# Kernel optimization log

Measured on AMD Instinct MI355X. Metric: run time of the kernel, lower is better.

## Reference

```python
import jax, jax.numpy as jnp
import numpy as np

B = 65536
DIM = 256       # latent_dim
N_EMBED = 1024  # codebook size


def setup_inputs() -> dict:
    key = jax.random.key(0)
    kx, ke = jax.random.split(key)
    x = jax.random.normal(kx, (B, DIM), dtype=jnp.float32)
    # rosinality Quantize stores codebook as embed[dim, n_embed]
    embed = jax.random.normal(ke, (DIM, N_EMBED), dtype=jnp.float32)
    return {"x": x, "embed": embed}


def reference(x, embed):
    # dist[b, k] = ||x_b||^2 - 2 x_b . e_k + ||e_k||^2  (negated for argmax in
    # the original; equivalent to argmin of the distance)
    x_sq = jnp.sum(x * x, axis=1, keepdims=True)            # [B, 1]
    e_sq = jnp.sum(embed * embed, axis=0, keepdims=True)    # [1, K]
    dist = x_sq - 2.0 * (x @ embed) + e_sq                  # [B, K]
    embed_ind = jnp.argmin(dist, axis=1)                    # [B] int
    # codebook lookup: embed.T is [K, dim]
    quantize = jnp.take(embed.T, embed_ind, axis=0)         # [B, dim]
    # commitment loss term
    diff = jnp.mean(jnp.square(jax.lax.stop_gradient(quantize) - x))
    # straight-through estimator
    quantize_st = x + jax.lax.stop_gradient(quantize - x)
    return quantize_st, diff, embed_ind
```

## Files before the change

kernel.cpp:

```cpp
#include <hip/hip_runtime.h>

#define NROWSQ   65536
#define NDIM     256
#define NCB      1024
#define DIFF_OFF 16777216
#define IDX_OFF  16777217

#define MARGIN_A 0.35f
#define MARGIN_A3 (MARGIN_A + 0.075f)
#define MARGIN_B 1.5e-3f
#define SCORE_SHIFT 384.0f

typedef __attribute__((ext_vector_type(8))) short s16x8;
typedef __attribute__((ext_vector_type(4))) float f32x4;

__device__ __forceinline__ unsigned short f2bf(float f) {
  union { float f; unsigned u; } v; v.f = f;
  return (unsigned short)((v.u + 0x7FFFu + ((v.u >> 16) & 1u)) >> 16);
}

__device__ __forceinline__ void gll16(const void* g, void* l) {
  __builtin_amdgcn_global_load_lds(
      (const __attribute__((address_space(1))) unsigned int*)g,
      (__attribute__((address_space(3))) unsigned int*)l, 16, 0, 0);
}

__device__ __forceinline__ void top2_merge(float& v1, int& i1, float& v2, int& i2,
                                           float ov1, int oi1, float ov2, int oi2) {
  if (ov1 > v1 || (ov1 == v1 && oi1 < i1)) {
    float nv2 = v1; int ni2 = i1;
    if (ov2 > nv2 || (ov2 == nv2 && oi2 < ni2)) { nv2 = ov2; ni2 = oi2; }
    v1 = ov1; i1 = oi1; v2 = nv2; i2 = ni2;
  } else if (ov1 > v2 || (ov1 == v2 && oi1 < i2)) {
    v2 = ov1; i2 = oi1;
  }
}

__device__ __forceinline__ float np_pairwise128(const float* p) {
  float r0 = p[0], r1 = p[1], r2 = p[2], r3 = p[3];
  float r4 = p[4], r5 = p[5], r6 = p[6], r7 = p[7];
  for (int i = 8; i < 128; i += 8) {
    r0 += p[i];     r1 += p[i + 1]; r2 += p[i + 2]; r3 += p[i + 3];
    r4 += p[i + 4]; r5 += p[i + 5]; r6 += p[i + 6]; r7 += p[i + 7];
  }
  return ((r0 + r1) + (r2 + r3)) + ((r4 + r5) + (r6 + r7));
}

__global__ void k0a_transpose(const float* __restrict__ E, float* __restrict__ embT,
                              unsigned short* __restrict__ cbT,
                              int* __restrict__ cnts, float* __restrict__ outDiff) {
  __shared__ float T[64][65];
  const int t = threadIdx.x;
  const int kbase = (blockIdx.x & 15) * 64;
  const int dbase = (blockIdx.x >> 4) * 64;
  if (blockIdx.x == 0) {
    if (t < 3) cnts[t] = 0;
    if (t == 3) *outDiff = 0.f;
  }
  #pragma unroll
  for (int i = 0; i < 4; ++i) {
    const int cid = i * 256 + t;
    const int dl = cid >> 4, kc = cid & 15;
    const float4 v = *(const float4*)(E + (size_t)(dbase + dl) * NCB + kbase + kc * 4);
    T[dl][kc * 4 + 0] = v.x; T[dl][kc * 4 + 1] = v.y;
    T[dl][kc * 4 + 2] = v.z; T[dl][kc * 4 + 3] = v.w;
  }
  __syncthreads();
  #pragma unroll
  for (int i = 0; i < 4; ++i) {
    const int cid = i * 256 + t;
    const int kl = cid >> 4, dc = cid & 15;
    float4 v;
    v.x = T[dc * 4 + 0][kl]; v.y = T[dc * 4 + 1][kl];
    v.z = T[dc * 4 + 2][kl]; v.w = T[dc * 4 + 3][kl];
    *(float4*)(embT + (size_t)(kbase + kl) * NDIM + dbase + dc * 4) = v;
    ushort4 b;
    b.x = f2bf(v.x); b.y = f2bf(v.y); b.z = f2bf(v.z); b.w = f2bf(v.w);
    const int dcol = dbase + dc * 4;
    const int sp = dcol ^ ((kl & 7) << 3);
    *(ushort4*)(cbT + (size_t)(kbase + kl) * NDIM + sp) = b;
  }
}

__global__ void k0b_esq(const float* __restrict__ embT, float* __restrict__ esq32,
                        float* __restrict__ esqs, float* __restrict__ esqr) {
  const int b = blockIdx.x, t = threadIdx.x;
  if (b < 128) {
    const int col = b * 8 + (t >> 5);
    const int l = t & 31;
    double s = 0.0;
    #pragma unroll
    for (int i = 0; i < 8; ++i) {
      const double v = (double)embT[(size_t)col * NDIM + l + i * 32];
      s += v * v;
    }
    #pragma unroll
    for (int m = 16; m >= 1; m >>= 1) s += __shfl_xor(s, m);
    if (l == 0) {
      esq32[col] = (float)(0.5 * s);
      esqs[col] = (float)(0.5 * s) - SCORE_SHIFT;
    }
  } else {
    __shared__ float Ls[16][260];
    const int col0 = (b - 128) * 16;
    #pragma unroll
    for (int i = 0; i < 4; ++i) {
      const int flat = i * 256 + t;
      const int row = flat >> 6, f4 = flat & 63;
      *(float4*)&Ls[row][f4 * 4] =
          *(const float4*)(embT + (size_t)(col0 + row) * NDIM + f4 * 4);
    }
    __syncthreads();
    if (t < 16) {
      float sr = 0.f;
      for (int d = 0; d < NDIM; ++d) {
        const float v = Ls[t][d];
        sr = sr + v * v;
      }
      esqr[col0 + t] = sr;
    }
  }
}

__global__ __launch_bounds__(256, 2) void k1_scores(
    const float* __restrict__ X, const unsigned short* __restrict__ cbT,
    const float* __restrict__ esqs, float* __restrict__ outIdx,
    int* __restrict__ cnts, int2* __restrict__ listP, int* __restrict__ listF) {
  __shared__ __align__(16) unsigned short Bs[2][64 * 256];
  __shared__ float esq_l[1024];
  const int t = threadIdx.x;
  const int lane = t & 63, w = t >> 6;
  const int l15 = lane & 15, quad = lane >> 4;
  const int rowbase = blockIdx.x * 128;
  const int swz = (l15 & 7) << 3;

  #pragma unroll
  for (int i = 0; i < 8; ++i)
    gll16(cbT + (size_t)(i * 256 + t) * 8, &Bs[0][(i * 256 + w * 64) * 8]);

  s16x8 afrag[2][8];
  #pragma unroll
  for (int m = 0; m < 2; ++m) {
    const float* xr = X + (size_t)(rowbase + w * 32 + m * 16 + l15) * NDIM;
    #pragma unroll
    for (int ks = 0; ks < 8; ++ks) {
      const float4 xa = *(const float4*)(xr + ks * 32 + quad * 8);
      const float4 xb = *(const float4*)(xr + ks * 32 + quad * 8 + 4);
      s16x8 a;
      a[0] = (short)f2bf(xa.x); a[1] = (short)f2bf(xa.y);
      a[2] = (short)f2bf(xa.z); a[3] = (short)f2bf(xa.w);
      a[4] = (short)f2bf(xb.x); a[5] = (short)f2bf(xb.y);
      a[6] = (short)f2bf(xb.z); a[7] = (short)f2bf(xb.w);
      afrag[m][ks] = a;
    }
  }

  {
    const float4 e4 = *(const float4*)(esqs + t * 4);
    *(float4*)(esq_l + t * 4) = e4;
  }

  int key1[2][4], key2[2][4], key3[2][4];
  #pragma unroll
  for (int m = 0; m < 2; ++m)
    #pragma unroll
    for (int r = 0; r < 4; ++r) { key1[m][r] = 0; key2[m][r] = 0; key3[m][r] = 0; }

  asm volatile("s_waitcnt vmcnt(0)" ::: "memory");
  __syncthreads();

  int cur = 0;
  for (int nt = 0; nt < 16; ++nt) {
    if (nt < 15) {
      const unsigned short* src = cbT + (size_t)(nt + 1) * (64 * 256);
      #pragma unroll
      for (int i = 0; i < 8; ++i)
        gll16(src + (size_t)(i * 256 + t) * 8, &Bs[cur ^ 1][(i * 256 + w * 64) * 8]);
    }

    f32x4 acc[2][4];
    #pragma unroll
    for (int m = 0; m < 2; ++m)
      #pragma unroll
      for (int s = 0; s < 4; ++s) acc[m][s] = (f32x4){0.f, 0.f, 0.f, 0.f};

    #pragma unroll
    for (int ks = 0; ks < 8; ++ks) {
      #pragma unroll
      for (int s = 0; s < 4; ++s) {
        const int us = (s * 16 + l15) * 256 + ((ks * 32 + quad * 8) ^ swz);
        const s16x8 bfr = *(const s16x8*)&Bs[cur][us];
        acc[0][s] = __builtin_amdgcn_mfma_f32_16x16x32_bf16(afrag[0][ks], bfr, acc[0][s], 0, 0, 0);
        acc[1][s] = __builtin_amdgcn_mfma_f32_16x16x32_bf16(afrag[1][ks], bfr, acc[1][s], 0, 0, 0);
      }
    }

    #pragma unroll
    for (int s = 0; s < 4; ++s) {
      const int lcol = nt * 64 + s * 16 + l15;
      const float eq = esq_l[lcol];
      const int suffix = 1023 - lcol;
      #pragma unroll
      for (int m = 0; m < 2; ++m)
        #pragma unroll
        for (int r = 0; r < 4; ++r) {
          float sc = acc[m][s][r] - eq;
          sc = fmaxf(sc, 1.0f);
          const int key = (__float_as_int(sc) & 0xFFFFFC00) | suffix;
          const int tt = min(key1[m][r], key);
          const int n3 = min(key2[m][r], tt);
          key1[m][r] = max(key1[m][r], key);
          key2[m][r] = max(key2[m][r], tt);
          key3[m][r] = max(key3[m][r], n3);
        }
    }

    asm volatile("s_waitcnt vmcnt(0)" ::: "memory");
    __syncthreads();
    cur ^= 1;
  }

  #pragma unroll
  for (int mask = 1; mask <= 8; mask <<= 1) {
    #pragma unroll
    for (int m = 0; m < 2; ++m)
      #pragma unroll
      for (int r = 0; r < 4; ++r) {
        const int a1 = key1[m][r], a2 = key2[m][r], a3 = key3[m][r];
        const int b1 = __shfl_xor(a1, mask);
        const int b2 = __shfl_xor(a2, mask);
        const int b3 = __shfl_xor(a3, mask);
        const int p = min(a1, b1);
        const int q = max(a2, b2);
        key1[m][r] = max(a1, b1);
        key2[m][r] = max(p, q);
        key3[m][r] = max(min(p, q), max(min(a2, b2), max(a3, b3)));
      }
  }

  if (l15 == 0) {
    #pragma unroll
    for (int m = 0; m < 2; ++m)
      #pragma unroll
      for (int r = 0; r < 4; ++r) {
        const int grow = rowbase + w * 32 + m * 16 + quad * 4 + r;
        const int k1v = key1[m][r], k2v = key2[m][r], k3v = key3[m][r];
        const int c1 = 1023 - (k1v & 1023);
        outIdx[grow] = (float)c1;
        const float g1 = __int_as_float(k1v & 0xFFFFFC00);
        const float g2 = __int_as_float(k2v & 0xFFFFFC00);
        if (g1 - g2 < MARGIN_A) {
          const float g3 = __int_as_float(k3v & 0xFFFFFC00);
          if (g1 - g3 > MARGIN_A3) {
            const int c2 = 1023 - (k2v & 1023);
            const int p = atomicAdd(&cnts[0], 1);
            listP[p] = make_int2(grow, c1 | (c2 << 16));
          } else {
            const int p = atomicAdd(&cnts[1], 1);
            listF[p] = grow;
          }
        }
      }
  }
}

__global__ __launch_bounds__(256) void k2p_pair(
    const float* __restrict__ X, const float* __restrict__ embT,
    const float* __restrict__ esq32, const int* __restrict__ cnts,
    const int2* __restrict__ listP, float* __restrict__ outIdx,
    int* __restrict__ cntB, int* __restrict__ listB) {
  const int cnt = cnts[0];
  for (int j = blockIdx.x * 256 + threadIdx.x; j < cnt; j += gridDim.x * 256) {
    const int2 e = listP[j];
    const int rid = e.x;
    const int c1 = e.y & 0xFFFF;
    const int c2 = ((unsigned)e.y) >> 16;
    const float* xr = X + (size_t)rid * NDIM;
    const float* e1 = embT + (size_t)c1 * NDIM;
    const float* e2 = embT + (size_t)c2 * NDIM;
    float a1 = 0.f, a2 = 0.f;
    #pragma unroll 4
    for (int dq = 0; dq < 64; ++dq) {
      const float4 x = *(const float4*)(xr + dq * 4);
      const float4 p = *(const float4*)(e1 + dq * 4);
      const float4 q = *(const float4*)(e2 + dq * 4);
      a1 = fmaf(x.x, p.x, a1); a1 = fmaf(x.y, p.y, a1);
      a1 = fmaf(x.z, p.z, a1); a1 = fmaf(x.w, p.w, a1);
      a2 = fmaf(x.x, q.x, a2); a2 = fmaf(x.y, q.y, a2);
      a2 = fmaf(x.z, q.z, a2); a2 = fmaf(x.w, q.w, a2);
    }
    const float s1 = a1 - esq32[c1];
    const float s2 = a2 - esq32[c2];
    float v1, v2; int i1;
    if (s1 > s2 || (s1 == s2 && c1 < c2)) { v1 = s1; i1 = c1; v2 = s2; }
    else                                  { v1 = s2; i1 = c2; v2 = s1; }
    outIdx[rid] = (float)i1;
    if (v1 - v2 < MARGIN_B) { const int p = atomicAdd(cntB, 1); listB[p] = rid; }
  }
}

__global__ __launch_bounds__(256) void k2a_refine(
    const float* __restrict__ X, const float* __restrict__ embT,
    const float* __restrict__ esq, const int* __restrict__ cnts,
    const int* __restrict__ listF, float4* __restrict__ part2) {
  __shared__ float Xs[8][NDIM];
  __shared__ float sv1[4][8], sv2[4][8];
  __shared__ int   si1[4][8], si2[4][8];
  const int t = threadIdx.x;
  const int lane = t & 63, w = t >> 6;
  const int split = blockIdx.x & 3;
  const int col = split * 256 + t;
  const int nslots = gridDim.x >> 2;
  const int cnt = cnts[1];
  const float eqc = esq[col];
  const float* er = embT + (size_t)col * NDIM;

  for (int base = (blockIdx.x >> 2) * 8; base < cnt; base += nslots * 8) {
    const int nrows = min(8, cnt - base);
    __syncthreads();
    for (int r = 0; r < 8; ++r) {
      const int rid = listF[base + min(r, nrows - 1)];
      Xs[r][t] = X[(size_t)rid * NDIM + t];
    }
    __syncthreads();

    float acc[8];
    #pragma unroll
    for (int r = 0; r < 8; ++r) acc[r] = 0.f;

    #pragma unroll 4
    for (int dq = 0; dq < 64; ++dq) {
      const float4 e = *(const float4*)(er + dq * 4);
      #pragma unroll
      for (int r = 0; r < 8; ++r) {
        const float4 x = *(const float4*)(&Xs[r][dq * 4]);
        float a = acc[r];
        a = fmaf(x.x, e.x, a);
        a = fmaf(x.y, e.y, a);
        a = fmaf(x.z, e.z, a);
        a = fmaf(x.w, e.w, a);
        acc[r] = a;
      }
    }

    #pragma unroll
    for (int r = 0; r < 8; ++r) {
      float v1 = acc[r] - eqc, v2 = -3.4e38f;
      int   i1 = col, i2 = 0x7fffffff;
      #pragma unroll
      for (int mask = 1; mask < 64; mask <<= 1) {
        const float ov1 = __shfl_xor(v1, mask); const int oi1 = __shfl_xor(i1, mask);
        const float ov2 = __shfl_xor(v2, mask); const int oi2 = __shfl_xor(i2, mask);
        top2_merge(v1, i1, v2, i2, ov1, oi1, ov2, oi2);
      }
      if (lane == 0) { sv1[w][r] = v1; si1[w][r] = i1; sv2[w][r] = v2; si2[w][r] = i2; }
    }
    __syncthreads();
    if (t < nrows) {
      const int r = t;
      float fv1 = sv1[0][r], fv2 = sv2[0][r]; int fi1 = si1[0][r], fi2 = si2[0][r];
      for (int ww = 1; ww < 4; ++ww)
        top2_merge(fv1, fi1, fv2, fi2, sv1[ww][r], si1[ww][r], sv2[ww][r], si2[ww][r]);
      part2[(size_t)split * NROWSQ + base + r] = make_float4(fv1, (float)fi1, fv2, (float)fi2);
    }
    __syncthreads();
  }
}

__global__ void k2m_merge(const float4* __restrict__ part2, const int* __restrict__ cnts,
                          const int* __restrict__ listF, float* __restrict__ outIdx,
                          int* __restrict__ cntB, int* __restrict__ listB) {
  const int cnt = cnts[1];
  for (int j = blockIdx.x * 256 + threadIdx.x; j < cnt; j += gridDim.x * 256) {
    const float4 a = part2[j];
    float v1 = a.x, v2 = a.z; int i1 = (int)a.y, i2 = (int)a.w;
    #pragma unroll
    for (int s = 1; s < 4; ++s) {
      const float4 b = part2[(size_t)s * NROWSQ + j];
      top2_merge(v1, i1, v2, i2, b.x, (int)b.y, b.z, (int)b.w);
    }
    const int rid = listF[j];
    outIdx[rid] = (float)i1;
    if (v1 - v2 < MARGIN_B) { const int p = atomicAdd(cntB, 1); listB[p] = rid; }
  }
}

__global__ __launch_bounds__(256) void k2b_mimic(
    const float* __restrict__ X, const float* __restrict__ embT,
    const float* __restrict__ esqr, const int* __restrict__ cntB,
    const int* __restrict__ listB, float* __restrict__ outIdx) {
  __shared__ float Xr[NDIM];
  __shared__ float Psq[NDIM];
  __shared__ float rv[256];
  __shared__ int ri[256];
  const int t = threadIdx.x;
  const int cnt = *cntB;
  for (int j = blockIdx.x; j < cnt; j += gridDim.x) {
    const int rid = listB[j];
    __syncthreads();
    {
      const float x = X[(size_t)rid * NDIM + t];
      Xr[t] = x;
      Psq[t] = x * x;
    }
    __syncthreads();
    const float x_sq = np_pairwise128(Psq) + np_pairwise128(Psq + 128);

    float best = 3.4e38f; int bidx = 0x7fffffff;
    #pragma unroll
    for (int c = 0; c < 4; ++c) {
      const int k = t + c * 256;
      const float* er = embT + (size_t)k * NDIM;
      float acc = 0.f;
      #pragma unroll 8
      for (int dq = 0; dq < 64; ++dq) {
        const float4 e = *(const float4*)(er + dq * 4);
        const float4 x = *(const float4*)(Xr + dq * 4);
        acc = fmaf(x.x, e.x, acc);
        acc = fmaf(x.y, e.y, acc);
        acc = fmaf(x.z, e.z, acc);
        acc = fmaf(x.w, e.w, acc);
      }
      const float dist = (x_sq - 2.0f * acc) + esqr[k];
      if (dist < best || (dist == best && k < bidx)) { best = dist; bidx = k; }
    }
    rv[t] = best; ri[t] = bidx;
    __syncthreads();
    for (int off = 128; off > 0; off >>= 1) {
      if (t < off) {
        if (rv[t + off] < rv[t] || (rv[t + off] == rv[t] && ri[t + off] < ri[t])) {
          rv[t] = rv[t + off]; ri[t] = ri[t + off];
        }
      }
      __syncthreads();
    }
    if (t == 0) outIdx[rid] = (float)ri[0];
  }
}

__global__ __launch_bounds__(256) void k4_outputs(
    const float* __restrict__ X, const float* __restrict__ embT,
    const float* __restrict__ idxF, float* __restrict__ outQ,
    float* __restrict__ outDiff) {
  const int t = threadIdx.x;
  const int lane = t & 63, w = t >> 6;
  const int W = blockIdx.x * 4 + w;
  float s = 0.f;
  #pragma unroll
  for (int i = 0; i < 8; ++i) {
    const int r = W + i * 8192;
    const int idx = (int)idxF[r];
    const float4 q = *(const float4*)(embT + idx * NDIM + lane * 4);
    const float4 x = *(const float4*)(X + (size_t)r * NDIM + lane * 4);
    *(float4*)(outQ + (size_t)r * NDIM + lane * 4) = q;
    const float dx = q.x - x.x, dy = q.y - x.y, dz = q.z - x.z, dw = q.w - x.w;
    s += dx * dx + dy * dy + dz * dz + dw * dw;
  }
  #pragma unroll
  for (int mask = 1; mask < 64; mask <<= 1) s += __shfl_xor(s, mask);
  __shared__ float bs[4];
  if (lane == 0) bs[w] = s;
  __syncthreads();
  if (t == 0)
    atomicAdd(outDiff, (bs[0] + bs[1] + bs[2] + bs[3]) * (1.0f / 16777216.0f));
}

extern "C" void kernel_launch(void* const* d_in, const int* in_sizes, int n_in,
                              void* d_out, int out_size, void* d_ws, size_t ws_size,
                              hipStream_t stream) {
  const float* X = (const float*)d_in[0];
  const float* E = (const float*)d_in[1];
  float* out = (float*)d_out;

  char* ws = (char*)d_ws;
  unsigned short* cbT = (unsigned short*)(ws + 0x000000);
  float*  embT  = (float*) (ws + 0x080000);
  float*  esq32 = (float*) (ws + 0x180000);
  float*  esqs  = (float*) (ws + 0x181000);
  float*  esqr  = (float*) (ws + 0x182000);
  int*  cnts  = (int*) (ws + 0x183000);
  int2* listP = (int2*)(ws + 0x183100);
  int*  listF = (int*) (ws + 0x203100);
  int*  listB = (int*) (ws + 0x243100);
  float4* part2 = (float4*)(ws + 0x283100);

  int* cntB = cnts + 2;

  float* outQ    = out;
  float* outDiff = out + DIFF_OFF;
  float* outIdx  = out + IDX_OFF;

  k0a_transpose<<<dim3(64), dim3(256), 0, stream>>>(E, embT, cbT, cnts, outDiff);
  k0b_esq<<<dim3(192), dim3(256), 0, stream>>>(embT, esq32, esqs, esqr);
  k1_scores<<<dim3(512), dim3(256), 0, stream>>>(X, cbT, esqs, outIdx, cnts, listP, listF);
  k2p_pair<<<dim3(256), dim3(256), 0, stream>>>(X, embT, esq32, cnts, listP,
                                                outIdx, cntB, listB);
  k2a_refine<<<dim3(2048), dim3(256), 0, stream>>>(X, embT, esq32, cnts, listF, part2);
  k2m_merge<<<dim3(64), dim3(256), 0, stream>>>(part2, cnts, listF, outIdx, cntB, listB);
  k2b_mimic<<<dim3(64), dim3(256), 0, stream>>>(X, embT, esqr, cntB, listB, outIdx);
  k4_outputs<<<dim3(2048), dim3(256), 0, stream>>>(X, embT, outIdx, outQ, outDiff);
}
```

Before: 303.1 us.

## Keep codebook quarter resident in LDS and split top-3 search across blocks

The score kernel now gives each 512-thread block a fixed 256-entry codebook quarter that it loads once into LDS. The block streams 1024 rows of X through it, so the per-tile double-buffered codebook streaming goes away. Each wave pair covers 64 codebook columns and writes partial top-3 keys per row to a scratch area borrowed from the quantize output. A new merge kernel combines the 16 partials and does the candidate classification. In exchange, X is read four times instead of once, extra partial-key traffic is added, and there is one more kernel launch.

```diff
diff --git a/kernel.cpp b/kernel.cpp
--- a/kernel.cpp
+++ b/kernel.cpp
@@ -122,61 +122,53 @@
   }
 }
 
-__global__ __launch_bounds__(256, 2) void k1_scores(
+__global__ __launch_bounds__(512, 2) void k1_scores(
     const float* __restrict__ X, const unsigned short* __restrict__ cbT,
-    const float* __restrict__ esqs, float* __restrict__ outIdx,
-    int* __restrict__ cnts, int2* __restrict__ listP, int* __restrict__ listF) {
-  __shared__ __align__(16) unsigned short Bs[2][64 * 256];
-  __shared__ float esq_l[1024];
+    const float* __restrict__ esqs, int4* __restrict__ part1) {
+  __shared__ __align__(16) unsigned short Bs[256 * 256];
+  __shared__ float esq_l[256];
   const int t = threadIdx.x;
   const int lane = t & 63, w = t >> 6;
   const int l15 = lane & 15, quad = lane >> 4;
-  const int rowbase = blockIdx.x * 128;
+  const int grp = blockIdx.x & 3;
+  const int slice = blockIdx.x >> 2;
+  const int roww = w >> 2;
+  const int cq = w & 3;
   const int swz = (l15 & 7) << 3;
 
+  const unsigned short* src = cbT + (size_t)grp * 256 * NDIM;
   #pragma unroll
-  for (int i = 0; i < 8; ++i)
-    gll16(cbT + (size_t)(i * 256 + t) * 8, &Bs[0][(i * 256 + w * 64) * 8]);
-
-  s16x8 afrag[2][8];
-  #pragma unroll
-  for (int m = 0; m < 2; ++m) {
-    const float* xr = X + (size_t)(rowbase + w * 32 + m * 16 + l15) * NDIM;
-    #pragma unroll
-    for (int ks = 0; ks < 8; ++ks) {
-      const float4 xa = *(const float4*)(xr + ks * 32 + quad * 8);
-      const float4 xb = *(const float4*)(xr + ks * 32 + quad * 8 + 4);
-      s16x8 a;
-      a[0] = (short)f2bf(xa.x); a[1] = (short)f2bf(xa.y);
-      a[2] = (short)f2bf(xa.z); a[3] = (short)f2bf(xa.w);
-      a[4] = (short)f2bf(xb.x); a[5] = (short)f2bf(xb.y);
-      a[6] = (short)f2bf(xb.z); a[7] = (short)f2bf(xb.w);
-      afrag[m][ks] = a;
-    }
-  }
-
-  {
-    const float4 e4 = *(const float4*)(esqs + t * 4);
-    *(float4*)(esq_l + t * 4) = e4;
-  }
-
-  int key1[2][4], key2[2][4], key3[2][4];
-  #pragma unroll
-  for (int m = 0; m < 2; ++m)
-    #pragma unroll
-    for (int r = 0; r < 4; ++r) { key1[m][r] = 0; key2[m][r] = 0; key3[m][r] = 0; }
-
+  for (int i = 0; i < 16; ++i)
+    gll16(src + (size_t)(i * 512 + t) * 8, &Bs[(i * 512 + w * 64) * 8]);
+  if (t < 256) esq_l[t] = esqs[grp * 256 + t];
   asm volatile("s_waitcnt vmcnt(0)" ::: "memory");
   __syncthreads();
 
-  int cur = 0;
-  for (int nt = 0; nt < 16; ++nt) {
-    if (nt < 15) {
-      const unsigned short* src = cbT + (size_t)(nt + 1) * (64 * 256);
-      #pragma unroll
-      for (int i = 0; i < 8; ++i)
-        gll16(src + (size_t)(i * 256 + t) * 8, &Bs[cur ^ 1][(i * 256 + w * 64) * 8]);
-    }
+  for (int j = 0; j < 16; ++j) {
+    const int rowbase = slice * 1024 + j * 64 + roww * 32;
+
+    float4 xa[2][8], xb[2][8];
+    #pragma unroll
+    for (int m = 0; m < 2; ++m) {
+      const float* xr = X + (size_t)(rowbase + m * 16 + l15) * NDIM;
+      #pragma unroll
+      for (int ks = 0; ks < 8; ++ks) {
+        xa[m][ks] = *(const float4*)(xr + ks * 32 + quad * 8);
+        xb[m][ks] = *(const float4*)(xr + ks * 32 + quad * 8 + 4);
+      }
+    }
+    s16x8 afrag[2][8];
+    #pragma unroll
+    for (int m = 0; m < 2; ++m)
+      #pragma unroll
+      for (int ks = 0; ks < 8; ++ks) {
+        s16x8 a;
+        a[0] = (short)f2bf(xa[m][ks].x); a[1] = (short)f2bf(xa[m][ks].y);
+        a[2] = (short)f2bf(xa[m][ks].z); a[3] = (short)f2bf(xa[m][ks].w);
+        a[4] = (short)f2bf(xb[m][ks].x); a[5] = (short)f2bf(xb[m][ks].y);
+        a[6] = (short)f2bf(xb[m][ks].z); a[7] = (short)f2bf(xb[m][ks].w);
+        afrag[m][ks] = a;
+      }
 
     f32x4 acc[2][4];
     #pragma unroll
@@ -188,18 +180,24 @@
     for (int ks = 0; ks < 8; ++ks) {
       #pragma unroll
       for (int s = 0; s < 4; ++s) {
-        const int us = (s * 16 + l15) * 256 + ((ks * 32 + quad * 8) ^ swz);
-        const s16x8 bfr = *(const s16x8*)&Bs[cur][us];
+        const int us = (cq * 64 + s * 16 + l15) * 256 + ((ks * 32 + quad * 8) ^ swz);
+        const s16x8 bfr = *(const s16x8*)&Bs[us];
         acc[0][s] = __builtin_amdgcn_mfma_f32_16x16x32_bf16(afrag[0][ks], bfr, acc[0][s], 0, 0, 0);
         acc[1][s] = __builtin_amdgcn_mfma_f32_16x16x32_bf16(afrag[1][ks], bfr, acc[1][s], 0, 0, 0);
       }
     }
 
+    int key1[2][4], key2[2][4], key3[2][4];
+    #pragma unroll
+    for (int m = 0; m < 2; ++m)
+      #pragma unroll
+      for (int r = 0; r < 4; ++r) { key1[m][r] = 0; key2[m][r] = 0; key3[m][r] = 0; }
+
     #pragma unroll
     for (int s = 0; s < 4; ++s) {
-      const int lcol = nt * 64 + s * 16 + l15;
+      const int lcol = cq * 64 + s * 16 + l15;
       const float eq = esq_l[lcol];
-      const int suffix = 1023 - lcol;
+      const int suffix = 1023 - (grp * 256 + lcol);
       #pragma unroll
       for (int m = 0; m < 2; ++m)
         #pragma unroll
@@ -215,52 +213,67 @@
         }
     }
 
-    asm volatile("s_waitcnt vmcnt(0)" ::: "memory");
-    __syncthreads();
-    cur ^= 1;
-  }
-
+    #pragma unroll
+    for (int mask = 1; mask <= 8; mask <<= 1) {
+      #pragma unroll
+      for (int m = 0; m < 2; ++m)
+        #pragma unroll
+        for (int r = 0; r < 4; ++r) {
+          const int a1 = key1[m][r], a2 = key2[m][r], a3 = key3[m][r];
+          const int b1 = __shfl_xor(a1, mask);
+          const int b2 = __shfl_xor(a2, mask);
+          const int b3 = __shfl_xor(a3, mask);
+          const int p = min(a1, b1);
+          const int q = max(a2, b2);
+          key1[m][r] = max(a1, b1);
+          key2[m][r] = max(p, q);
+          key3[m][r] = max(min(p, q), max(min(a2, b2), max(a3, b3)));
+        }
+    }
+
+    if (l15 == 0) {
+      const size_t plane = (size_t)(grp * 4 + cq) * NROWSQ;
+      #pragma unroll
+      for (int m = 0; m < 2; ++m)
+        #pragma unroll
+        for (int r = 0; r < 4; ++r) {
+          const int grow = rowbase + m * 16 + quad * 4 + r;
+          part1[plane + grow] = make_int4(key1[m][r], key2[m][r], key3[m][r], 0);
+        }
+    }
+  }
+}
+
+__global__ void k1m_merge(const int4* __restrict__ part1, float* __restrict__ outIdx,
+                          int* __restrict__ cnts, int2* __restrict__ listP,
+                          int* __restrict__ listF) {
+  const int row = blockIdx.x * 256 + threadIdx.x;
+  const int4 a0 = part1[row];
+  int k1 = a0.x, k2 = a0.y, k3 = a0.z;
   #pragma unroll
-  for (int mask = 1; mask <= 8; mask <<= 1) {
-    #pragma unroll
-    for (int m = 0; m < 2; ++m)
-      #pragma unroll
-      for (int r = 0; r < 4; ++r) {
-        const int a1 = key1[m][r], a2 = key2[m][r], a3 = key3[m][r];
-        const int b1 = __shfl_xor(a1, mask);
-        const int b2 = __shfl_xor(a2, mask);
-        const int b3 = __shfl_xor(a3, mask);
-        const int p = min(a1, b1);
-        const int q = max(a2, b2);
-        key1[m][r] = max(a1, b1);
-        key2[m][r] = max(p, q);
-        key3[m][r] = max(min(p, q), max(min(a2, b2), max(a3, b3)));
-      }
-  }
-
-  if (l15 == 0) {
-    #pragma unroll
-    for (int m = 0; m < 2; ++m)
-      #pragma unroll
-      for (int r = 0; r < 4; ++r) {
-        const int grow = rowbase + w * 32 + m * 16 + quad * 4 + r;
-        const int k1v = key1[m][r], k2v = key2[m][r], k3v = key3[m][r];
-        const int c1 = 1023 - (k1v & 1023);
-        outIdx[grow] = (float)c1;
-        const float g1 = __int_as_float(k1v & 0xFFFFFC00);
-        const float g2 = __int_as_float(k2v & 0xFFFFFC00);
-        if (g1 - g2 < MARGIN_A) {
-          const float g3 = __int_as_float(k3v & 0xFFFFFC00);
-          if (g1 - g3 > MARGIN_A3) {
-            const int c2 = 1023 - (k2v & 1023);
-            const int p = atomicAdd(&cnts[0], 1);
-            listP[p] = make_int2(grow, c1 | (c2 << 16));
-          } else {
-            const int p = atomicAdd(&cnts[1], 1);
-            listF[p] = grow;
-          }
-        }
-      }
+  for (int g = 1; g < 16; ++g) {
+    const int4 b = part1[(size_t)g * NROWSQ + row];
+    const int p = min(k1, b.x);
+    const int q = max(k2, b.y);
+    const int n1 = max(k1, b.x);
+    const int n2 = max(p, q);
+    const int n3 = max(min(p, q), max(min(k2, b.y), max(k3, b.z)));
+    k1 = n1; k2 = n2; k3 = n3;
+  }
+  const int c1 = 1023 - (k1 & 1023);
+  outIdx[row] = (float)c1;
+  const float g1 = __int_as_float(k1 & 0xFFFFFC00);
+  const float g2 = __int_as_float(k2 & 0xFFFFFC00);
+  if (g1 - g2 < MARGIN_A) {
+    const float g3 = __int_as_float(k3 & 0xFFFFFC00);
+    if (g1 - g3 > MARGIN_A3) {
+      const int c2 = 1023 - (k2 & 1023);
+      const int p = atomicAdd(&cnts[0], 1);
+      listP[p] = make_int2(row, c1 | (c2 << 16));
+    } else {
+      const int p = atomicAdd(&cnts[1], 1);
+      listF[p] = row;
+    }
   }
 }
 
@@ -490,9 +503,12 @@
   float* outDiff = out + DIFF_OFF;
   float* outIdx  = out + IDX_OFF;
 
+  int4* part1 = (int4*)outQ;
+
   k0a_transpose<<<dim3(64), dim3(256), 0, stream>>>(E, embT, cbT, cnts, outDiff);
   k0b_esq<<<dim3(192), dim3(256), 0, stream>>>(embT, esq32, esqs, esqr);
-  k1_scores<<<dim3(512), dim3(256), 0, stream>>>(X, cbT, esqs, outIdx, cnts, listP, listF);
+  k1_scores<<<dim3(256), dim3(512), 0, stream>>>(X, cbT, esqs, part1);
+  k1m_merge<<<dim3(256), dim3(256), 0, stream>>>(part1, outIdx, cnts, listP, listF);
   k2p_pair<<<dim3(256), dim3(256), 0, stream>>>(X, embT, esq32, cnts, listP,
                                                 outIdx, cntB, listB);
   k2a_refine<<<dim3(2048), dim3(256), 0, stream>>>(X, embT, esq32, cnts, listF, part2);
```

Measured after the change: 374.0 us. +23.4%, slower.

## Shrink k1 tiles to 64 rows and single-buffer LDS for higher occupancy

Applied to the files above, without the earlier changes.

The scoring kernel now handles 16 rows per wave (64 per block) instead of 32, halving accumulator and A-fragment registers. The codebook LDS buffer becomes single-buffered, which halves shared memory so four blocks can fit per CU. The grid doubles to 1024 blocks. In exchange, the prefetch of the next codebook tile no longer overlaps the MFMA work: each tile is loaded synchronously between two barriers. Each codebook tile is also reused by half as many rows, so total codebook traffic from L2 doubles.

```diff
diff --git a/kernel.cpp b/kernel.cpp
--- a/kernel.cpp
+++ b/kernel.cpp
@@ -122,26 +122,25 @@
   }
 }
 
-__global__ __launch_bounds__(256, 2) void k1_scores(
+__global__ __launch_bounds__(256, 4) void k1_scores(
     const float* __restrict__ X, const unsigned short* __restrict__ cbT,
     const float* __restrict__ esqs, float* __restrict__ outIdx,
     int* __restrict__ cnts, int2* __restrict__ listP, int* __restrict__ listF) {
-  __shared__ __align__(16) unsigned short Bs[2][64 * 256];
+  __shared__ __align__(16) unsigned short Bs[64 * 256];
   __shared__ float esq_l[1024];
   const int t = threadIdx.x;
   const int lane = t & 63, w = t >> 6;
   const int l15 = lane & 15, quad = lane >> 4;
-  const int rowbase = blockIdx.x * 128;
+  const int rowbase = blockIdx.x * 64 + w * 16;
   const int swz = (l15 & 7) << 3;
 
   #pragma unroll
   for (int i = 0; i < 8; ++i)
-    gll16(cbT + (size_t)(i * 256 + t) * 8, &Bs[0][(i * 256 + w * 64) * 8]);
-
-  s16x8 afrag[2][8];
-  #pragma unroll
-  for (int m = 0; m < 2; ++m) {
-    const float* xr = X + (size_t)(rowbase + w * 32 + m * 16 + l15) * NDIM;
+    gll16(cbT + (size_t)(i * 256 + t) * 8, &Bs[(i * 256 + w * 64) * 8]);
+
+  s16x8 afrag[8];
+  {
+    const float* xr = X + (size_t)(rowbase + l15) * NDIM;
     #pragma unroll
     for (int ks = 0; ks < 8; ++ks) {
       const float4 xa = *(const float4*)(xr + ks * 32 + quad * 8);
@@ -151,7 +150,7 @@
       a[2] = (short)f2bf(xa.z); a[3] = (short)f2bf(xa.w);
       a[4] = (short)f2bf(xb.x); a[5] = (short)f2bf(xb.y);
       a[6] = (short)f2bf(xb.z); a[7] = (short)f2bf(xb.w);
-      afrag[m][ks] = a;
+      afrag[ks] = a;
     }
   }
 
@@ -160,38 +159,25 @@
     *(float4*)(esq_l + t * 4) = e4;
   }
 
-  int key1[2][4], key2[2][4], key3[2][4];
-  #pragma unroll
-  for (int m = 0; m < 2; ++m)
-    #pragma unroll
-    for (int r = 0; r < 4; ++r) { key1[m][r] = 0; key2[m][r] = 0; key3[m][r] = 0; }
+  int key1[4], key2[4], key3[4];
+  #pragma unroll
+  for (int r = 0; r < 4; ++r) { key1[r] = 0; key2[r] = 0; key3[r] = 0; }
 
   asm volatile("s_waitcnt vmcnt(0)" ::: "memory");
   __syncthreads();
 
-  int cur = 0;
   for (int nt = 0; nt < 16; ++nt) {
-    if (nt < 15) {
-      const unsigned short* src = cbT + (size_t)(nt + 1) * (64 * 256);
-      #pragma unroll
-      for (int i = 0; i < 8; ++i)
-        gll16(src + (size_t)(i * 256 + t) * 8, &Bs[cur ^ 1][(i * 256 + w * 64) * 8]);
-    }
-
-    f32x4 acc[2][4];
-    #pragma unroll
-    for (int m = 0; m < 2; ++m)
-      #pragma unroll
-      for (int s = 0; s < 4; ++s) acc[m][s] = (f32x4){0.f, 0.f, 0.f, 0.f};
+    f32x4 acc[4];
+    #pragma unroll
+    for (int s = 0; s < 4; ++s) acc[s] = (f32x4){0.f, 0.f, 0.f, 0.f};
 
     #pragma unroll
     for (int ks = 0; ks < 8; ++ks) {
       #pragma unroll
       for (int s = 0; s < 4; ++s) {
         const int us = (s * 16 + l15) * 256 + ((ks * 32 + quad * 8) ^ swz);
-        const s16x8 bfr = *(const s16x8*)&Bs[cur][us];
-        acc[0][s] = __builtin_amdgcn_mfma_f32_16x16x32_bf16(afrag[0][ks], bfr, acc[0][s], 0, 0, 0);
-        acc[1][s] = __builtin_amdgcn_mfma_f32_16x16x32_bf16(afrag[1][ks], bfr, acc[1][s], 0, 0, 0);
+        const s16x8 bfr = *(const s16x8*)&Bs[us];
+        acc[s] = __builtin_amdgcn_mfma_f32_16x16x32_bf16(afrag[ks], bfr, acc[s], 0, 0, 0);
       }
     }
 
@@ -201,66 +187,66 @@
       const float eq = esq_l[lcol];
       const int suffix = 1023 - lcol;
       #pragma unroll
-      for (int m = 0; m < 2; ++m)
-        #pragma unroll
-        for (int r = 0; r < 4; ++r) {
-          float sc = acc[m][s][r] - eq;
-          sc = fmaxf(sc, 1.0f);
-          const int key = (__float_as_int(sc) & 0xFFFFFC00) | suffix;
-          const int tt = min(key1[m][r], key);
-          const int n3 = min(key2[m][r], tt);
-          key1[m][r] = max(key1[m][r], key);
-          key2[m][r] = max(key2[m][r], tt);
-          key3[m][r] = max(key3[m][r], n3);
+      for (int r = 0; r < 4; ++r) {
+        float sc = acc[s][r] - eq;
+        sc = fmaxf(sc, 1.0f);
+        const int key = (__float_as_int(sc) & 0xFFFFFC00) | suffix;
+        const int tt = min(key1[r], key);
+        const int n3 = min(key2[r], tt);
+        key1[r] = max(key1[r], key);
+        key2[r] = max(key2[r], tt);
+        key3[r] = max(key3[r], n3);
+      }
+    }
+
+    __syncthreads();
+    if (nt < 15) {
+      const unsigned short* src = cbT + (size_t)(nt + 1) * (64 * 256);
+      #pragma unroll
+      for (int i = 0; i < 8; ++i)
+        gll16(src + (size_t)(i * 256 + t) * 8, &Bs[(i * 256 + w * 64) * 8]);
+      asm volatile("s_waitcnt vmcnt(0)" ::: "memory");
+    }
+    __syncthreads();
+  }
+
+  #pragma unroll
+  for (int mask = 1; mask <= 8; mask <<= 1) {
+    #pragma unroll
+    for (int r = 0; r < 4; ++r) {
+      const int a1 = key1[r], a2 = key2[r], a3 = key3[r];
+      const int b1 = __shfl_xor(a1, mask);
+      const int b2 = __shfl_xor(a2, mask);
+      const int b3 = __shfl_xor(a3, mask);
+      const int p = min(a1, b1);
+      const int q = max(a2, b2);
+      key1[r] = max(a1, b1);
+      key2[r] = max(p, q);
+      key3[r] = max(min(p, q), max(min(a2, b2), max(a3, b3)));
+    }
+  }
+
+  if (l15 == 0) {
+    #pragma unroll
+    for (int r = 0; r < 4; ++r) {
+      const int grow = rowbase + quad * 4 + r;
+      const int k1v = key1[r], k2v = key2[r], k3v = key3[r];
+      const int c1 = 1023 - (k1v & 1023);
+      outIdx[grow] = (float)c1;
+      const float g1 = __int_as_float(k1v & 0xFFFFFC00);
+      const float g2 = __int_as_float(k2v & 0xFFFFFC00);
+      if (g1 - g2 < MARGIN_A) {
+        const float g3 = __int_as_float(k3v & 0xFFFFFC00);
+        if (g1 - g3 > MARGIN_A3) {
+          const int c2 = 1023 - (k2v & 1023);
+          const int p = atomicAdd(&cnts[0], 1);
+          listP[p] = make_int2(grow, c1 | (c2 << 16));
+        } else {
+          const int p = atomicAdd(&cnts[1], 1);
+          listF[p] = grow;
         }
-    }
-
-    asm volatile("s_waitcnt vmcnt(0)" ::: "memory");
-    __syncthreads();
-    cur ^= 1;
-  }
-
-  #pragma unroll
-  for (int mask = 1; mask <= 8; mask <<= 1) {
-    #pragma unroll
-    for (int m = 0; m < 2; ++m)
-      #pragma unroll
-      for (int r = 0; r < 4; ++r) {
-        const int a1 = key1[m][r], a2 = key2[m][r], a3 = key3[m][r];
-        const int b1 = __shfl_xor(a1, mask);
-        const int b2 = __shfl_xor(a2, mask);
-        const int b3 = __shfl_xor(a3, mask);
-        const int p = min(a1, b1);
-        const int q = max(a2, b2);
-        key1[m][r] = max(a1, b1);
-        key2[m][r] = max(p, q);
-        key3[m][r] = max(min(p, q), max(min(a2, b2), max(a3, b3)));
-      }
-  }
-
-  if (l15 == 0) {
-    #pragma unroll
-    for (int m = 0; m < 2; ++m)
-      #pragma unroll
-      for (int r = 0; r < 4; ++r) {
-        const int grow = rowbase + w * 32 + m * 16 + quad * 4 + r;
-        const int k1v = key1[m][r], k2v = key2[m][r], k3v = key3[m][r];
-        const int c1 = 1023 - (k1v & 1023);
-        outIdx[grow] = (float)c1;
-        const float g1 = __int_as_float(k1v & 0xFFFFFC00);
-        const float g2 = __int_as_float(k2v & 0xFFFFFC00);
-        if (g1 - g2 < MARGIN_A) {
-          const float g3 = __int_as_float(k3v & 0xFFFFFC00);
-          if (g1 - g3 > MARGIN_A3) {
-            const int c2 = 1023 - (k2v & 1023);
-            const int p = atomicAdd(&cnts[0], 1);
-            listP[p] = make_int2(grow, c1 | (c2 << 16));
-          } else {
-            const int p = atomicAdd(&cnts[1], 1);
-            listF[p] = grow;
-          }
-        }
-      }
+      }
+    }
   }
 }
 
@@ -492,7 +478,7 @@
 
   k0a_transpose<<<dim3(64), dim3(256), 0, stream>>>(E, embT, cbT, cnts, outDiff);
   k0b_esq<<<dim3(192), dim3(256), 0, stream>>>(embT, esq32, esqs, esqr);
-  k1_scores<<<dim3(512), dim3(256), 0, stream>>>(X, cbT, esqs, outIdx, cnts, listP, listF);
+  k1_scores<<<dim3(1024), dim3(256), 0, stream>>>(X, cbT, esqs, outIdx, cnts, listP, listF);
   k2p_pair<<<dim3(256), dim3(256), 0, stream>>>(X, embT, esq32, cnts, listP,
                                                 outIdx, cntB, listB);
   k2a_refine<<<dim3(2048), dim3(256), 0, stream>>>(X, embT, esq32, cnts, listF, part2);
```

After: 302.8 us. About the same (-0.1%).
